# Kernel optimization log

Measured on AMD Instinct MI355X. Metric: run time of the kernel, lower is better.

## Reference

```python
import jax, jax.numpy as jnp
import numpy as np

B, L, E, H = 2, 2048, 1024, 16
Dh = E // H  # 64


def setup_inputs() -> dict:
    key = jax.random.key(0)
    ks = jax.random.split(key, 12)
    s = 0.02  # realistic init scale for weights
    inp = {
        "x_q": jax.random.normal(ks[0], (B, L, E), jnp.float32),
        "x_k": jax.random.normal(ks[1], (B, L, E), jnp.float32),
        "x_v": jax.random.normal(ks[2], (B, L, E), jnp.float32),
        # causal mask, broadcast over batch and heads: [1,1,Lq,Lk]
        "mask": jnp.tril(jnp.ones((L, L), jnp.int32))[None, None],
        "Wq": jax.random.normal(ks[3], (E, E), jnp.float32) * s,
        "bq": jnp.zeros((E,), jnp.float32),
        "Wk": jax.random.normal(ks[4], (E, E), jnp.float32) * s,
        "bk": jnp.zeros((E,), jnp.float32),
        "Wv": jax.random.normal(ks[5], (E, E), jnp.float32) * s,
        "bv": jnp.zeros((E,), jnp.float32),
        "Wo": jax.random.normal(ks[6], (E, E), jnp.float32) * s,
        "bo": jnp.zeros((E,), jnp.float32),
    }
    return inp


def reference(x_q, x_k, x_v, mask, Wq, bq, Wk, bk, Wv, bv, Wo, bo):
    N, Lq, _ = x_q.shape
    Lk = x_k.shape[1]
    # Linear projections (torch Linear: x @ W.T + b), split heads -> [B,H,L,Dh]
    q = (x_q @ Wq.T + bq).reshape(N, Lq, H, Dh).transpose(0, 2, 1, 3)
    k = (x_k @ Wk.T + bk).reshape(N, Lk, H, Dh).transpose(0, 2, 1, 3)
    v = (x_v @ Wv.T + bv).reshape(N, Lk, H, Dh).transpose(0, 2, 1, 3)
    # naive SDPA: full [B,H,Lq,Lk] score matrix, exactly as the source module
    scores = jnp.einsum("bhqd,bhkd->bhqk", q, k) / jnp.sqrt(jnp.float32(Dh))
    scores = jnp.where(mask == 0, jnp.float32(-1e9), scores)
    attn = jax.nn.softmax(scores, axis=-1)
    out = jnp.einsum("bhqk,bhkd->bhqd", attn, v)
    out = out.transpose(0, 2, 1, 3).reshape(N, Lq, E)
    return out @ Wo.T + bo
```

## Files before the change

kernel.cpp:

```cpp
#include <hip/hip_runtime.h>
#include <stdint.h>
#include <stddef.h>


#define AS1 __attribute__((address_space(1)))
#define AS3 __attribute__((address_space(3)))

typedef __attribute__((ext_vector_type(8))) __bf16 bf16x8;
typedef __attribute__((ext_vector_type(8))) unsigned short u16x8;
typedef __attribute__((ext_vector_type(4))) unsigned short u16x4;
typedef __attribute__((ext_vector_type(4))) float f32x4;
typedef __attribute__((ext_vector_type(2))) unsigned int u32x2;

#define QSCALE 0.18033688011112042f

static __device__ __forceinline__ unsigned short f2bf(float f) {
  unsigned int u = __builtin_bit_cast(unsigned int, f);
  u += 0x7fffu + ((u >> 16) & 1u);
  return (unsigned short)(u >> 16);
}
static __device__ __forceinline__ unsigned int pkbf(float lo, float hi) {
  return __builtin_amdgcn_perm(__builtin_bit_cast(unsigned int, hi),
                               __builtin_bit_cast(unsigned int, lo), 0x07060302u);
}
static __device__ __forceinline__ void g2l16(const unsigned short* g, unsigned short* l) {
  __builtin_amdgcn_global_load_lds((AS1 void*)g, (AS3 void*)l, 16, 0, 0);
}
static __device__ __forceinline__ float fexp2(float x) {
  return __builtin_amdgcn_exp2f(x);
}

__global__ __launch_bounds__(256) void cvt_kernel(
    const float* __restrict__ s0, const float* __restrict__ s1,
    const float* __restrict__ s2, const float* __restrict__ s3,
    const float* __restrict__ s4, const float* __restrict__ s5,
    const float* __restrict__ s6,
    unsigned short* __restrict__ d0, unsigned short* __restrict__ d1,
    unsigned short* __restrict__ d2, unsigned short* __restrict__ d3,
    unsigned short* __restrict__ d4, unsigned short* __restrict__ d5,
    unsigned short* __restrict__ d6)
{
  const int z = blockIdx.z;
  const float* s; unsigned short* d; int n;
  switch (z) {
    case 0: s = s0; d = d0; n = 4194304; break;
    case 1: s = s1; d = d1; n = 4194304; break;
    case 2: s = s2; d = d2; n = 4194304; break;
    case 3: s = s3; d = d3; n = 1048576; break;
    case 4: s = s4; d = d4; n = 1048576; break;
    case 5: s = s5; d = d5; n = 1048576; break;
    default: s = s6; d = d6; n = 1048576; break;
  }
  int i = (blockIdx.x * 256 + threadIdx.x) * 8;
  if (i >= n) return;
  f32x4 a = *(const f32x4*)(s + i);
  f32x4 b = *(const f32x4*)(s + i + 4);
  u16x8 r;
  r[0] = f2bf(a[0]); r[1] = f2bf(a[1]); r[2] = f2bf(a[2]); r[3] = f2bf(a[3]);
  r[4] = f2bf(b[0]); r[5] = f2bf(b[1]); r[6] = f2bf(b[2]); r[7] = f2bf(b[3]);
  *(u16x8*)(d + i) = r;
}

template<int BM, int BN>
static __device__ __forceinline__ void gemm_bt(
    const unsigned short* __restrict__ A,
    const unsigned short* __restrict__ Bw,
    const float* __restrict__ bias,
    unsigned short* __restrict__ outb,
    float* __restrict__ outf,
    int K, int N, int mode, float oscale)
{
  constexpr int MT = BM / 32;
  constexpr int NT = BN / 32;
  __shared__ __align__(16) unsigned short As[2][BM * 32];
  __shared__ __align__(16) unsigned short Bs[2][BN * 32];

  const int t    = threadIdx.x;
  const int lane = t & 63;
  const int w    = t >> 6;
  const int quad = lane >> 4;
  const int l15  = lane & 15;
  const int wm   = (w >> 1) * (BM / 2);
  const int wn   = (w & 1) * (BN / 2);
  const int m0   = blockIdx.x * BM;
  const int n0   = blockIdx.y * BN;

  f32x4 acc[MT][NT];
  const f32x4 zero = {0.f, 0.f, 0.f, 0.f};
#pragma unroll
  for (int mt = 0; mt < MT; ++mt)
#pragma unroll
    for (int nt = 0; nt < NT; ++nt) acc[mt][nt] = zero;

  auto stage = [&](int buf, int k0) {
#pragma unroll
    for (int i = 0; i < BM / 64; ++i) {
      int c = t + i * 256;
      int row = c >> 2, sl = c & 3;
      int g = sl ^ ((row >> 1) & 3);
      g2l16(A + (size_t)(m0 + row) * K + (k0 + g * 8), &As[buf][c * 8]);
    }
#pragma unroll
    for (int i = 0; i < BN / 64; ++i) {
      int c = t + i * 256;
      int row = c >> 2, sl = c & 3;
      int g = sl ^ ((row >> 1) & 3);
      g2l16(Bw + (size_t)(n0 + row) * K + (k0 + g * 8), &Bs[buf][c * 8]);
    }
  };

  stage(0, 0);
  const int nk = K >> 5;
  for (int kt = 0; kt < nk; ++kt) {
    __syncthreads();
    if (kt + 1 < nk) stage((kt + 1) & 1, (kt + 1) * 32);
    const int b = kt & 1;

    bf16x8 af[MT], bfr[NT];
#pragma unroll
    for (int mt = 0; mt < MT; ++mt) {
      int r = wm + mt * 16 + l15;
      af[mt] = *(const bf16x8*)(&As[b][r * 32 + ((quad ^ ((r >> 1) & 3)) * 8)]);
    }
#pragma unroll
    for (int nt = 0; nt < NT; ++nt) {
      int r = wn + nt * 16 + l15;
      bfr[nt] = *(const bf16x8*)(&Bs[b][r * 32 + ((quad ^ ((r >> 1) & 3)) * 8)]);
    }
#pragma unroll
    for (int mt = 0; mt < MT; ++mt)
#pragma unroll
      for (int nt = 0; nt < NT; ++nt)
        acc[mt][nt] = __builtin_amdgcn_mfma_f32_16x16x32_bf16(af[mt], bfr[nt], acc[mt][nt], 0, 0, 0);
  }

#pragma unroll
  for (int nt = 0; nt < NT; ++nt) {
    int n = n0 + wn + nt * 16 + l15;
    float bv = bias[n];
#pragma unroll
    for (int mt = 0; mt < MT; ++mt) {
#pragma unroll
      for (int r = 0; r < 4; ++r) {
        int m = m0 + wm + mt * 16 + quad * 4 + r;
        float val = (acc[mt][nt][r] + bv) * oscale;
        if (mode == 0) {
          outf[(size_t)m * N + n] = val;
        } else {
          int b2 = m >> 11, l = m & 2047, h = n >> 6, d = n & 63;
          size_t idx;
          if (mode == 1) idx = ((size_t)(b2 * 16 + h) * 2048 + l) * 64 + d;
          else           idx = ((size_t)(b2 * 16 + h) * 64 + d) * 2048 + l;
          outb[idx] = f2bf(val);
        }
      }
    }
  }
}

__global__ __launch_bounds__(256, 5) void proj_kernel(
    const unsigned short* __restrict__ xq, const unsigned short* __restrict__ xk,
    const unsigned short* __restrict__ xv,
    const unsigned short* __restrict__ Wq, const float* __restrict__ bq,
    const unsigned short* __restrict__ Wk, const float* __restrict__ bk,
    const unsigned short* __restrict__ Wv, const float* __restrict__ bv,
    unsigned short* __restrict__ Qws, unsigned short* __restrict__ Kws,
    unsigned short* __restrict__ Vtws)
{
  int z = blockIdx.z;
  const unsigned short* A = (z == 0) ? xq : (z == 1) ? xk : xv;
  const unsigned short* W = (z == 0) ? Wq : (z == 1) ? Wk : Wv;
  const float* bias       = (z == 0) ? bq : (z == 1) ? bk : bv;
  unsigned short* out     = (z == 0) ? Qws : (z == 1) ? Kws : Vtws;
  float oscale            = (z == 0) ? QSCALE : 1.0f;
  gemm_bt<128, 64>(A, W, bias, out, nullptr, 1024, 1024, (z == 2) ? 2 : 1, oscale);
}

__global__ __launch_bounds__(256, 4) void oproj_kernel(
    const unsigned short* __restrict__ Ain, const unsigned short* __restrict__ Wo,
    const float* __restrict__ bo, float* __restrict__ out)
{
  gemm_bt<64, 128>(Ain, Wo, bo, nullptr, out, 1024, 1024, 0, 1.0f);
}

__global__ __launch_bounds__(256, 2) void flash_kernel(
    const unsigned short* __restrict__ Q,
    const unsigned short* __restrict__ Km,
    const unsigned short* __restrict__ Vt,
    unsigned short* __restrict__ Ao)
{
  __shared__ __align__(16) unsigned short Ks[2][64 * 64];
  __shared__ __align__(16) unsigned short Vs[2][64 * 64];
  __shared__ __align__(16) unsigned short PsA[4][16 * 64];
  __shared__ __align__(16) unsigned short PsB[4][16 * 64];

  const int t    = threadIdx.x;
  const int lane = t & 63;
  const int w    = t >> 6;
  const int quad = lane >> 4;
  const int l15  = lane & 15;
  const int pi   = blockIdx.x;
  const int bh   = blockIdx.y;
  const int qtA  = 31 - pi;
  const int qtB  = pi;

  const unsigned short* Qb = Q  + (size_t)bh * 2048 * 64;
  const unsigned short* Kb = Km + (size_t)bh * 2048 * 64;
  const unsigned short* Vb = Vt + (size_t)bh * 64 * 2048;
  const int bb = bh >> 4, hh = bh & 15;

  const f32x4 zero = {0.f, 0.f, 0.f, 0.f};

  bf16x8 qfA[2], qfB[2];
#pragma unroll
  for (int s = 0; s < 2; ++s) {
    qfA[s] = *(const bf16x8*)(Qb + (size_t)(qtA * 64 + w * 16 + l15) * 64 + s * 32 + quad * 8);
    qfB[s] = *(const bf16x8*)(Qb + (size_t)(qtB * 64 + w * 16 + l15) * 64 + s * 32 + quad * 8);
  }

  f32x4 oA[4], oB[4];
#pragma unroll
  for (int mt = 0; mt < 4; ++mt) { oA[mt] = zero; oB[mt] = zero; }
  float lA = 0.f, lB = 0.f;

  auto stage = [&](int buf, int kv0) {
#pragma unroll
    for (int i = 0; i < 2; ++i) {
      int c = t + i * 256;
      int row = c >> 3, sl = c & 7;
      int g = sl ^ (row & 7);
      g2l16(Kb + (size_t)(kv0 + row) * 64 + g * 8, &Ks[buf][c * 8]);
      g2l16(Vb + (size_t)row * 2048 + kv0 + g * 8, &Vs[buf][c * 8]);
    }
  };

  stage(0, 0);

  const int pwr = l15 * 64 + (quad & 1) * 4;
  const int pu0 = quad >> 1;
  const int ph  = l15 & 7;

#pragma unroll 1
  for (int it = 0; it <= qtA; ++it) {
    __syncthreads();
    const int cur = it & 1;
    if (it < qtA) stage(cur ^ 1, (it + 1) * 64);
    const bool doB = (it <= qtB);

    bf16x8 kf[4][2];
#pragma unroll
    for (int mt = 0; mt < 4; ++mt) {
      int kv = mt * 16 + l15;
#pragma unroll
      for (int s = 0; s < 2; ++s)
        kf[mt][s] = *(const bf16x8*)(&Ks[cur][kv * 64 + (((s * 4 + quad) ^ (kv & 7)) * 8)]);
    }

    f32x4 sA[4], sB[4];
#pragma unroll
    for (int mt = 0; mt < 4; ++mt) {
      f32x4 z = zero;
      z = __builtin_amdgcn_mfma_f32_16x16x32_bf16(kf[mt][0], qfA[0], z, 0, 0, 0);
      z = __builtin_amdgcn_mfma_f32_16x16x32_bf16(kf[mt][1], qfA[1], z, 0, 0, 0);
      sA[mt] = z;
    }
    if (doB) {
#pragma unroll
      for (int mt = 0; mt < 4; ++mt) {
        f32x4 z = zero;
        z = __builtin_amdgcn_mfma_f32_16x16x32_bf16(kf[mt][0], qfB[0], z, 0, 0, 0);
        z = __builtin_amdgcn_mfma_f32_16x16x32_bf16(kf[mt][1], qfB[1], z, 0, 0, 0);
        sB[mt] = z;
      }
    }

    const int qloc = w * 16 + l15;
    if (it == qtA) {
#pragma unroll
      for (int mt = 0; mt < 4; ++mt)
#pragma unroll
        for (int r = 0; r < 4; ++r)
          if (mt * 16 + quad * 4 + r > qloc) sA[mt][r] = -30000.f;
    }
    if (it == qtB) {
#pragma unroll
      for (int mt = 0; mt < 4; ++mt)
#pragma unroll
        for (int r = 0; r < 4; ++r)
          if (mt * 16 + quad * 4 + r > qloc) sB[mt][r] = -30000.f;
    }

#pragma unroll
    for (int mt = 0; mt < 4; ++mt) {
      float p0 = fexp2(sA[mt][0]), p1 = fexp2(sA[mt][1]);
      float p2 = fexp2(sA[mt][2]), p3 = fexp2(sA[mt][3]);
      lA += (p0 + p1) + (p2 + p3);
      u32x2 pk = {pkbf(p0, p1), pkbf(p2, p3)};
      *(u32x2*)(&PsA[w][pwr + (((mt * 2 + pu0) ^ ph) * 8)]) = pk;
    }
    if (doB) {
#pragma unroll
      for (int mt = 0; mt < 4; ++mt) {
        float p0 = fexp2(sB[mt][0]), p1 = fexp2(sB[mt][1]);
        float p2 = fexp2(sB[mt][2]), p3 = fexp2(sB[mt][3]);
        lB += (p0 + p1) + (p2 + p3);
        u32x2 pk = {pkbf(p0, p1), pkbf(p2, p3)};
        *(u32x2*)(&PsB[w][pwr + (((mt * 2 + pu0) ^ ph) * 8)]) = pk;
      }
    }

    bf16x8 pfA[2], pfB[2];
#pragma unroll
    for (int s = 0; s < 2; ++s)
      pfA[s] = *(const bf16x8*)(&PsA[w][l15 * 64 + (((s * 4 + quad) ^ ph) * 8)]);
    if (doB) {
#pragma unroll
      for (int s = 0; s < 2; ++s)
        pfB[s] = *(const bf16x8*)(&PsB[w][l15 * 64 + (((s * 4 + quad) ^ ph) * 8)]);
    }
#pragma unroll
    for (int mt = 0; mt < 4; ++mt) {
      int dd = mt * 16 + l15;
      bf16x8 vf0 = *(const bf16x8*)(&Vs[cur][dd * 64 + (((quad)     ^ (dd & 7)) * 8)]);
      bf16x8 vf1 = *(const bf16x8*)(&Vs[cur][dd * 64 + (((4 + quad) ^ (dd & 7)) * 8)]);
      oA[mt] = __builtin_amdgcn_mfma_f32_16x16x32_bf16(vf0, pfA[0], oA[mt], 0, 0, 0);
      oA[mt] = __builtin_amdgcn_mfma_f32_16x16x32_bf16(vf1, pfA[1], oA[mt], 0, 0, 0);
      if (doB) {
        oB[mt] = __builtin_amdgcn_mfma_f32_16x16x32_bf16(vf0, pfB[0], oB[mt], 0, 0, 0);
        oB[mt] = __builtin_amdgcn_mfma_f32_16x16x32_bf16(vf1, pfB[1], oB[mt], 0, 0, 0);
      }
    }
  }

#pragma unroll
  for (int half = 0; half < 2; ++half) {
    float lp = half ? lB : lA;
    lp += __shfl_xor(lp, 16, 64);
    lp += __shfl_xor(lp, 32, 64);
    float inv = 1.0f / lp;
    const int qt = half ? qtB : qtA;
    const f32x4* o = half ? oB : oA;
    size_t rowbase = ((size_t)(bb * 2048 + qt * 64 + w * 16 + l15)) * 1024 + hh * 64;
#pragma unroll
    for (int mt = 0; mt < 4; ++mt) {
      u16x4 v;
#pragma unroll
      for (int r = 0; r < 4; ++r) v[r] = f2bf(o[mt][r] * inv);
      *(u16x4*)(Ao + rowbase + mt * 16 + quad * 4) = v;
    }
  }
}

extern "C" void kernel_launch(void* const* d_in, const int* in_sizes, int n_in,
                              void* d_out, int out_size, void* d_ws, size_t ws_size,
                              hipStream_t stream)
{
  (void)in_sizes; (void)n_in; (void)out_size; (void)ws_size;

  const float* xq = (const float*)d_in[0];
  const float* xk = (const float*)d_in[1];
  const float* xv = (const float*)d_in[2];
  const float* Wq = (const float*)d_in[4];
  const float* bq = (const float*)d_in[5];
  const float* Wk = (const float*)d_in[6];
  const float* bk = (const float*)d_in[7];
  const float* Wv = (const float*)d_in[8];
  const float* bv = (const float*)d_in[9];
  const float* Wo = (const float*)d_in[10];
  const float* bo = (const float*)d_in[11];

  const size_t NX = (size_t)4194304;
  const size_t NW = (size_t)1048576;
  unsigned short* Qws  = (unsigned short*)d_ws;
  unsigned short* Kws  = Qws + NX;
  unsigned short* Vtws = Kws + NX;
  unsigned short* xqbf = Vtws + NX;
  unsigned short* xkbf = xqbf + NX;
  unsigned short* xvbf = xkbf + NX;
  unsigned short* Wqbf = xvbf + NX;
  unsigned short* Wkbf = Wqbf + NW;
  unsigned short* Wvbf = Wkbf + NW;
  unsigned short* Wobf = Wvbf + NW;
  unsigned short* Aws  = xqbf;

  dim3 gc(2048, 1, 7);
  cvt_kernel<<<gc, 256, 0, stream>>>(xq, xk, xv, Wq, Wk, Wv, Wo,
                                     xqbf, xkbf, xvbf, Wqbf, Wkbf, Wvbf, Wobf);
  dim3 gp(32, 16, 3);
  proj_kernel<<<gp, 256, 0, stream>>>(xqbf, xkbf, xvbf, Wqbf, bq, Wkbf, bk,
                                      Wvbf, bv, Qws, Kws, Vtws);
  dim3 gf(16, 32, 1);
  flash_kernel<<<gf, 256, 0, stream>>>(Qws, Kws, Vtws, Aws);
  dim3 go(64, 8, 1);
  oproj_kernel<<<go, 256, 0, stream>>>(Aws, Wobf, bo, (float*)d_out);
}
```

Baseline: 234.0 us.

## Fuse fp32-to-bf16 conversion into GEMM staging and drop the cvt kernel

Removes the separate conversion kernel and instead loads fp32 inputs and weights directly in the GEMM tile staging, packing them to bf16 in registers before storing to LDS. This removes a full read/write pass over about 19M elements and one launch. The projection tile is enlarged to 128x128 with lower occupancy. The cost is that fp32 staging goes through registers instead of asynchronous global-to-LDS loads, reads twice the bytes per tile, and re-reads and re-converts each operand once per block tile.

Result: slower. 265.0 us (+13.2%).

```diff
diff --git a/kernel.cpp b/kernel.cpp
--- a/kernel.cpp
+++ b/kernel.cpp
@@ -11,6 +11,7 @@
 typedef __attribute__((ext_vector_type(4))) unsigned short u16x4;
 typedef __attribute__((ext_vector_type(4))) float f32x4;
 typedef __attribute__((ext_vector_type(2))) unsigned int u32x2;
+typedef __attribute__((ext_vector_type(4))) unsigned int u32x4;
 
 #define QSCALE 0.18033688011112042f
 
@@ -29,42 +30,20 @@
 static __device__ __forceinline__ float fexp2(float x) {
   return __builtin_amdgcn_exp2f(x);
 }
-
-__global__ __launch_bounds__(256) void cvt_kernel(
-    const float* __restrict__ s0, const float* __restrict__ s1,
-    const float* __restrict__ s2, const float* __restrict__ s3,
-    const float* __restrict__ s4, const float* __restrict__ s5,
-    const float* __restrict__ s6,
-    unsigned short* __restrict__ d0, unsigned short* __restrict__ d1,
-    unsigned short* __restrict__ d2, unsigned short* __restrict__ d3,
-    unsigned short* __restrict__ d4, unsigned short* __restrict__ d5,
-    unsigned short* __restrict__ d6)
-{
-  const int z = blockIdx.z;
-  const float* s; unsigned short* d; int n;
-  switch (z) {
-    case 0: s = s0; d = d0; n = 4194304; break;
-    case 1: s = s1; d = d1; n = 4194304; break;
-    case 2: s = s2; d = d2; n = 4194304; break;
-    case 3: s = s3; d = d3; n = 1048576; break;
-    case 4: s = s4; d = d4; n = 1048576; break;
-    case 5: s = s5; d = d5; n = 1048576; break;
-    default: s = s6; d = d6; n = 1048576; break;
-  }
-  int i = (blockIdx.x * 256 + threadIdx.x) * 8;
-  if (i >= n) return;
-  f32x4 a = *(const f32x4*)(s + i);
-  f32x4 b = *(const f32x4*)(s + i + 4);
-  u16x8 r;
-  r[0] = f2bf(a[0]); r[1] = f2bf(a[1]); r[2] = f2bf(a[2]); r[3] = f2bf(a[3]);
-  r[4] = f2bf(b[0]); r[5] = f2bf(b[1]); r[6] = f2bf(b[2]); r[7] = f2bf(b[3]);
-  *(u16x8*)(d + i) = r;
-}
-
-template<int BM, int BN>
+static __device__ __forceinline__ void stage8f(const float* __restrict__ p,
+                                               unsigned short* __restrict__ dst) {
+  f32x4 a = *(const f32x4*)p;
+  f32x4 b = *(const f32x4*)(p + 4);
+  u32x4 pk;
+  pk[0] = pkbf(a[0], a[1]); pk[1] = pkbf(a[2], a[3]);
+  pk[2] = pkbf(b[0], b[1]); pk[3] = pkbf(b[2], b[3]);
+  *(u32x4*)dst = pk;
+}
+
+template<int BM, int BN, bool AF32, bool BF32>
 static __device__ __forceinline__ void gemm_bt(
-    const unsigned short* __restrict__ A,
-    const unsigned short* __restrict__ Bw,
+    const void* __restrict__ Av,
+    const void* __restrict__ Bv,
     const float* __restrict__ bias,
     unsigned short* __restrict__ outb,
     float* __restrict__ outf,
@@ -85,6 +64,11 @@
   const int m0   = blockIdx.x * BM;
   const int n0   = blockIdx.y * BN;
 
+  const float* Af          = (const float*)Av;
+  const unsigned short* Ab = (const unsigned short*)Av;
+  const float* Bf          = (const float*)Bv;
+  const unsigned short* Bb = (const unsigned short*)Bv;
+
   f32x4 acc[MT][NT];
   const f32x4 zero = {0.f, 0.f, 0.f, 0.f};
 #pragma unroll
@@ -98,14 +82,16 @@
       int c = t + i * 256;
       int row = c >> 2, sl = c & 3;
       int g = sl ^ ((row >> 1) & 3);
-      g2l16(A + (size_t)(m0 + row) * K + (k0 + g * 8), &As[buf][c * 8]);
+      if (AF32) stage8f(Af + (size_t)(m0 + row) * K + (k0 + g * 8), &As[buf][c * 8]);
+      else      g2l16(Ab + (size_t)(m0 + row) * K + (k0 + g * 8), &As[buf][c * 8]);
     }
 #pragma unroll
     for (int i = 0; i < BN / 64; ++i) {
       int c = t + i * 256;
       int row = c >> 2, sl = c & 3;
       int g = sl ^ ((row >> 1) & 3);
-      g2l16(Bw + (size_t)(n0 + row) * K + (k0 + g * 8), &Bs[buf][c * 8]);
+      if (BF32) stage8f(Bf + (size_t)(n0 + row) * K + (k0 + g * 8), &Bs[buf][c * 8]);
+      else      g2l16(Bb + (size_t)(n0 + row) * K + (k0 + g * 8), &Bs[buf][c * 8]);
     }
   };
 
@@ -158,29 +144,30 @@
   }
 }
 
-__global__ __launch_bounds__(256, 5) void proj_kernel(
-    const unsigned short* __restrict__ xq, const unsigned short* __restrict__ xk,
-    const unsigned short* __restrict__ xv,
-    const unsigned short* __restrict__ Wq, const float* __restrict__ bq,
-    const unsigned short* __restrict__ Wk, const float* __restrict__ bk,
-    const unsigned short* __restrict__ Wv, const float* __restrict__ bv,
+__global__ __launch_bounds__(256, 3) void proj_kernel(
+    const float* __restrict__ xq, const float* __restrict__ xk,
+    const float* __restrict__ xv,
+    const float* __restrict__ Wq, const float* __restrict__ bq,
+    const float* __restrict__ Wk, const float* __restrict__ bk,
+    const float* __restrict__ Wv, const float* __restrict__ bv,
     unsigned short* __restrict__ Qws, unsigned short* __restrict__ Kws,
     unsigned short* __restrict__ Vtws)
 {
   int z = blockIdx.z;
-  const unsigned short* A = (z == 0) ? xq : (z == 1) ? xk : xv;
-  const unsigned short* W = (z == 0) ? Wq : (z == 1) ? Wk : Wv;
-  const float* bias       = (z == 0) ? bq : (z == 1) ? bk : bv;
-  unsigned short* out     = (z == 0) ? Qws : (z == 1) ? Kws : Vtws;
-  float oscale            = (z == 0) ? QSCALE : 1.0f;
-  gemm_bt<128, 64>(A, W, bias, out, nullptr, 1024, 1024, (z == 2) ? 2 : 1, oscale);
+  const float* A      = (z == 0) ? xq : (z == 1) ? xk : xv;
+  const float* W      = (z == 0) ? Wq : (z == 1) ? Wk : Wv;
+  const float* bias   = (z == 0) ? bq : (z == 1) ? bk : bv;
+  unsigned short* out = (z == 0) ? Qws : (z == 1) ? Kws : Vtws;
+  float oscale        = (z == 0) ? QSCALE : 1.0f;
+  gemm_bt<128, 128, true, true>(A, W, bias, out, nullptr, 1024, 1024,
+                                (z == 2) ? 2 : 1, oscale);
 }
 
 __global__ __launch_bounds__(256, 4) void oproj_kernel(
-    const unsigned short* __restrict__ Ain, const unsigned short* __restrict__ Wo,
+    const unsigned short* __restrict__ Ain, const float* __restrict__ Wo,
     const float* __restrict__ bo, float* __restrict__ out)
 {
-  gemm_bt<64, 128>(Ain, Wo, bo, nullptr, out, 1024, 1024, 0, 1.0f);
+  gemm_bt<64, 128, false, true>(Ain, Wo, bo, nullptr, out, 1024, 1024, 0, 1.0f);
 }
 
 __global__ __launch_bounds__(256, 2) void flash_kernel(
@@ -370,27 +357,16 @@
   const float* bo = (const float*)d_in[11];
 
   const size_t NX = (size_t)4194304;
-  const size_t NW = (size_t)1048576;
   unsigned short* Qws  = (unsigned short*)d_ws;
   unsigned short* Kws  = Qws + NX;
   unsigned short* Vtws = Kws + NX;
-  unsigned short* xqbf = Vtws + NX;
-  unsigned short* xkbf = xqbf + NX;
-  unsigned short* xvbf = xkbf + NX;
-  unsigned short* Wqbf = xvbf + NX;
-  unsigned short* Wkbf = Wqbf + NW;
-  unsigned short* Wvbf = Wkbf + NW;
-  unsigned short* Wobf = Wvbf + NW;
-  unsigned short* Aws  = xqbf;
-
-  dim3 gc(2048, 1, 7);
-  cvt_kernel<<<gc, 256, 0, stream>>>(xq, xk, xv, Wq, Wk, Wv, Wo,
-                                     xqbf, xkbf, xvbf, Wqbf, Wkbf, Wvbf, Wobf);
-  dim3 gp(32, 16, 3);
-  proj_kernel<<<gp, 256, 0, stream>>>(xqbf, xkbf, xvbf, Wqbf, bq, Wkbf, bk,
-                                      Wvbf, bv, Qws, Kws, Vtws);
+  unsigned short* Aws  = Vtws + NX;
+
+  dim3 gp(32, 8, 3);
+  proj_kernel<<<gp, 256, 0, stream>>>(xq, xk, xv, Wq, bq, Wk, bk, Wv, bv,
+                                      Qws, Kws, Vtws);
   dim3 gf(16, 32, 1);
   flash_kernel<<<gf, 256, 0, stream>>>(Qws, Kws, Vtws, Aws);
   dim3 go(64, 8, 1);
-  oproj_kernel<<<go, 256, 0, stream>>>(Aws, Wobf, bo, (float*)d_out);
-}
+  oproj_kernel<<<go, 256, 0, stream>>>(Aws, Wo, bo, (float*)d_out);
+}
```
